# Performance work log

Hardware: AMD Instinct MI355X
Metric: run time of the kernel (lower is better)

The kernel has to match this reference:

```python
import jax, jax.numpy as jnp
import numpy as np

B, S, H, U = 32, 4096, 512, 512


def setup_inputs() -> dict:
    key = jax.random.key(0)
    ks = jax.random.split(key, 6)
    scale = 1.0 / np.sqrt(H)
    return {
        "query": jax.random.normal(ks[0], (B, H), dtype=jnp.float32),
        "values": jax.random.normal(ks[1], (B, S, H), dtype=jnp.float32),
        "W1": jax.random.normal(ks[2], (H, U), dtype=jnp.float32) * scale,
        "b1": jnp.zeros((U,), dtype=jnp.float32),
        "W2": jax.random.normal(ks[3], (H, U), dtype=jnp.float32) * scale,
        "b2": jnp.zeros((U,), dtype=jnp.float32),
        "va": jax.random.normal(ks[4], (U, 1), dtype=jnp.float32) * (1.0 / np.sqrt(U)),
        "bva": jnp.zeros((1,), dtype=jnp.float32),
    }


def reference(query, values, W1, b1, W2, b2, va, bva):
    # query: [B, H] -> [B, 1, U]; values: [B, S, H] -> [B, S, U]
    q_proj = jnp.einsum('bh,hu->bu', query, W1) + b1           # [B, U]
    v_proj = jnp.einsum('bsh,hu->bsu', values, W2) + b2        # [B, S, U]
    scores = jnp.einsum('bsu,uo->bso', jnp.tanh(q_proj[:, None, :] + v_proj), va) + bva  # [B, S, 1]
    attention_weights = jax.nn.softmax(scores, axis=1)         # [B, S, 1]
    context_vector = jnp.sum(attention_weights * values, axis=1)  # [B, H]
    return attention_weights, context_vector
```

## Files before the change

kernel.cpp:

```cpp
#include <hip/hip_runtime.h>
#include <hip/hip_bf16.h>
#include <stdint.h>

#define B_SZ 32
#define S_SZ 4096
#define H_SZ 512
#define U_SZ 512

typedef __attribute__((ext_vector_type(8))) _Float16 half8;
typedef __attribute__((ext_vector_type(4))) float floatx4;

__global__ __launch_bounds__(256) void prep_kernel(
    const float* __restrict__ W2, _Float16* __restrict__ W2s,
    float* __restrict__ qpb2, float* __restrict__ ctx)
{
    const int t = threadIdx.x;
    const int bid = blockIdx.x;
    const int i = bid * 256 + t;
    const int k = i >> 9, n = i & 511;
    W2s[(k >> 5) * 16384 + ((k >> 3) & 3) * 4096 + n * 8 + (k & 7)] =
        (_Float16)W2[i];
    if (bid < 64) qpb2[i] = 0.0f;
    else if (bid < 128) ctx[(bid - 64) * 256 + t] = 0.0f;
}

__global__ __launch_bounds__(256) void qproj_kernel(
    const float* __restrict__ query, const float* __restrict__ W1,
    const float* __restrict__ b1, const float* __restrict__ b2,
    float* __restrict__ qpb2)
{
    const int b = blockIdx.x, uc = blockIdx.y, ks = blockIdx.z;
    const int u = uc * 256 + threadIdx.x;
    const float* q  = query + b * H_SZ + ks * 64;
    const float* Wp = W1 + (size_t)(ks * 64) * U_SZ + u;
    float a0 = 0.f, a1 = 0.f, a2 = 0.f, a3 = 0.f;
    for (int k = 0; k < 64; k += 4) {
        a0 = fmaf(q[k],     Wp[(size_t)k * U_SZ],       a0);
        a1 = fmaf(q[k + 1], Wp[(size_t)(k + 1) * U_SZ], a1);
        a2 = fmaf(q[k + 2], Wp[(size_t)(k + 2) * U_SZ], a2);
        a3 = fmaf(q[k + 3], Wp[(size_t)(k + 3) * U_SZ], a3);
    }
    float acc = (a0 + a1) + (a2 + a3);
    if (ks == 0) acc += b1[u] + b2[u];
    atomicAdd(&qpb2[b * U_SZ + u], acc);
}

__global__ __launch_bounds__(256, 2) void scores_kernel(
    const float* __restrict__ values, const _Float16* __restrict__ W2s,
    const float* __restrict__ qpb2, const float* __restrict__ va,
    const float* __restrict__ bva, float* __restrict__ scores)
{
    __shared__ float red[256];

    const int t  = threadIdx.x;
    const int w  = t >> 6;
    const int l  = t & 63;
    const int c  = l & 15;
    const int g4 = l >> 4;
    const int m0 = blockIdx.x * 64;
    const int b  = m0 >> 12;

    floatx4 acc[4][8];
#pragma unroll
    for (int mt = 0; mt < 4; ++mt)
#pragma unroll
        for (int nt = 0; nt < 8; ++nt) acc[mt][nt] = (floatx4)(0.0f);

    const float* Ab = values + (size_t)(m0 + c) * H_SZ + g4 * 8;
    const _Float16* Bb = W2s + g4 * 4096 + (w * 128 + c) * 8;

    float4 an0[4], an1[4];
#pragma unroll
    for (int mt = 0; mt < 4; ++mt) {
        const float* ap = Ab + (size_t)(mt * 16) * H_SZ;
        an0[mt] = *(const float4*)(ap);
        an1[mt] = *(const float4*)(ap + 4);
    }
    half8 af[4];
#pragma unroll
    for (int mt = 0; mt < 4; ++mt) {
        half8 a;
        a[0] = (_Float16)an0[mt].x; a[1] = (_Float16)an0[mt].y;
        a[2] = (_Float16)an0[mt].z; a[3] = (_Float16)an0[mt].w;
        a[4] = (_Float16)an1[mt].x; a[5] = (_Float16)an1[mt].y;
        a[6] = (_Float16)an1[mt].z; a[7] = (_Float16)an1[mt].w;
        af[mt] = a;
    }

    for (int kb = 0; kb < 16; ++kb) {
        half8 bf[8];
        const _Float16* Bp = Bb + kb * 16384;
#pragma unroll
        for (int nt = 0; nt < 8; ++nt)
            bf[nt] = *(const half8*)(Bp + nt * 128);
        if (kb < 15) {
#pragma unroll
            for (int mt = 0; mt < 4; ++mt) {
                const float* ap = Ab + (size_t)(mt * 16) * H_SZ + (kb + 1) * 32;
                an0[mt] = *(const float4*)(ap);
                an1[mt] = *(const float4*)(ap + 4);
            }
        }
#pragma unroll
        for (int nt = 0; nt < 8; ++nt)
#pragma unroll
            for (int mt = 0; mt < 4; ++mt)
                acc[mt][nt] = __builtin_amdgcn_mfma_f32_16x16x32_f16(
                    af[mt], bf[nt], acc[mt][nt], 0, 0, 0);
        if (kb < 15) {
#pragma unroll
            for (int mt = 0; mt < 4; ++mt) {
                half8 a;
                a[0] = (_Float16)an0[mt].x; a[1] = (_Float16)an0[mt].y;
                a[2] = (_Float16)an0[mt].z; a[3] = (_Float16)an0[mt].w;
                a[4] = (_Float16)an1[mt].x; a[5] = (_Float16)an1[mt].y;
                a[6] = (_Float16)an1[mt].z; a[7] = (_Float16)an1[mt].w;
                af[mt] = a;
            }
        }
    }

    float qv2[8], vv[8], vv2[8];
#pragma unroll
    for (int nt = 0; nt < 8; ++nt) {
        const int n = w * 128 + nt * 16 + c;
        const float q = qpb2[b * U_SZ + n];
        const float v = va[n];
        qv2[nt] = 2.0f * q;
        vv[nt] = v;
        vv2[nt] = 2.0f * v;
    }
#pragma unroll
    for (int mt = 0; mt < 4; ++mt) {
#pragma unroll
        for (int r = 0; r < 4; ++r) {
            float p = 0.0f;
#pragma unroll
            for (int nt = 0; nt < 8; ++nt) {
                const float ex = __expf(fmaf(acc[mt][nt][r], 2.0f, qv2[nt]));
                const float rc = __builtin_amdgcn_rcpf(ex + 1.0f);
                p = fmaf(-vv2[nt], rc, p + vv[nt]);
            }
            p += __shfl_xor(p, 1);
            p += __shfl_xor(p, 2);
            p += __shfl_xor(p, 4);
            p += __shfl_xor(p, 8);
            if (c == 0) red[(mt * 16 + g4 * 4 + r) * 4 + w] = p;
        }
    }
    __syncthreads();
    if (t < 64)
        scores[m0 + t] = *bva + red[t * 4 + 0] + red[t * 4 + 1] +
                         red[t * 4 + 2] + red[t * 4 + 3];
}

__global__ __launch_bounds__(1024) void sredux_kernel(
    const float* __restrict__ scores, float* __restrict__ ML)
{
    __shared__ float red[16];
    __shared__ float s_max;
    const int b = blockIdx.x;
    const int t = threadIdx.x;
    float4 v = *(const float4*)(scores + b * S_SZ + t * 4);
    float m = fmaxf(fmaxf(v.x, v.y), fmaxf(v.z, v.w));
#pragma unroll
    for (int o = 32; o > 0; o >>= 1) m = fmaxf(m, __shfl_xor(m, o));
    if ((t & 63) == 0) red[t >> 6] = m;
    __syncthreads();
    if (t == 0) {
        float mm = red[0];
        for (int i = 1; i < 16; ++i) mm = fmaxf(mm, red[i]);
        s_max = mm;
    }
    __syncthreads();
    const float mm = s_max;
    float s = __expf(v.x - mm) + __expf(v.y - mm) +
              __expf(v.z - mm) + __expf(v.w - mm);
#pragma unroll
    for (int o = 32; o > 0; o >>= 1) s += __shfl_xor(s, o);
    if ((t & 63) == 0) red[t >> 6] = s;
    __syncthreads();
    if (t == 0) {
        float ss = 0.0f;
        for (int i = 0; i < 16; ++i) ss += red[i];
        ML[b * 2] = mm;
        ML[b * 2 + 1] = ss;
    }
}

__global__ __launch_bounds__(256) void context_kernel(
    const float* __restrict__ values, const float* __restrict__ scores,
    const float* __restrict__ ML, float* __restrict__ out)
{
    __shared__ float wl[128];
    __shared__ __align__(16) float part[4][64][4];
    const int ss = blockIdx.x, hc = blockIdx.y, b = blockIdx.z;
    const int t = threadIdx.x;
    const float M = ML[b * 2];
    const float rL = 1.0f / ML[b * 2 + 1];
    if (t < 32) {
        float4 sv = *(const float4*)(scores + b * S_SZ + ss * 128 + t * 4);
        float4 wv;
        wv.x = __expf(sv.x - M) * rL; wv.y = __expf(sv.y - M) * rL;
        wv.z = __expf(sv.z - M) * rL; wv.w = __expf(sv.w - M) * rL;
        *(float4*)&wl[t * 4] = wv;
        if (hc == 0)
            *(float4*)(out + b * S_SZ + ss * 128 + t * 4) = wv;
    }
    __syncthreads();

    const int l = t & 63, g = t >> 6;
    const float* vp = values + ((size_t)b * S_SZ + ss * 128 + g * 32) * H_SZ +
                      hc * 256 + l * 4;
    float4 a0 = {0,0,0,0}, a1 = {0,0,0,0}, a2 = {0,0,0,0}, a3 = {0,0,0,0};
    for (int i = 0; i < 32; i += 4) {
        const float w0 = wl[g * 32 + i];
        const float w1 = wl[g * 32 + i + 1];
        const float w2 = wl[g * 32 + i + 2];
        const float w3 = wl[g * 32 + i + 3];
        float4 v0 = *(const float4*)(vp + (size_t)(i)     * H_SZ);
        float4 v1 = *(const float4*)(vp + (size_t)(i + 1) * H_SZ);
        float4 v2 = *(const float4*)(vp + (size_t)(i + 2) * H_SZ);
        float4 v3 = *(const float4*)(vp + (size_t)(i + 3) * H_SZ);
        a0.x = fmaf(w0, v0.x, a0.x); a0.y = fmaf(w0, v0.y, a0.y);
        a0.z = fmaf(w0, v0.z, a0.z); a0.w = fmaf(w0, v0.w, a0.w);
        a1.x = fmaf(w1, v1.x, a1.x); a1.y = fmaf(w1, v1.y, a1.y);
        a1.z = fmaf(w1, v1.z, a1.z); a1.w = fmaf(w1, v1.w, a1.w);
        a2.x = fmaf(w2, v2.x, a2.x); a2.y = fmaf(w2, v2.y, a2.y);
        a2.z = fmaf(w2, v2.z, a2.z); a2.w = fmaf(w2, v2.w, a2.w);
        a3.x = fmaf(w3, v3.x, a3.x); a3.y = fmaf(w3, v3.y, a3.y);
        a3.z = fmaf(w3, v3.z, a3.z); a3.w = fmaf(w3, v3.w, a3.w);
    }
    a0.x += a1.x + a2.x + a3.x; a0.y += a1.y + a2.y + a3.y;
    a0.z += a1.z + a2.z + a3.z; a0.w += a1.w + a2.w + a3.w;
    *(float4*)&part[g][l][0] = a0;
    __syncthreads();
    if (t < 64) {
        float4 sa = *(float4*)&part[0][t][0];
#pragma unroll
        for (int gg = 1; gg < 4; ++gg) {
            float4 p = *(float4*)&part[gg][t][0];
            sa.x += p.x; sa.y += p.y; sa.z += p.z; sa.w += p.w;
        }
        float* ctx = out + B_SZ * S_SZ;
        const int hh = hc * 256 + t * 4;
        atomicAdd(&ctx[b * H_SZ + hh + 0], sa.x);
        atomicAdd(&ctx[b * H_SZ + hh + 1], sa.y);
        atomicAdd(&ctx[b * H_SZ + hh + 2], sa.z);
        atomicAdd(&ctx[b * H_SZ + hh + 3], sa.w);
    }
}

extern "C" void kernel_launch(void* const* d_in, const int* in_sizes, int n_in,
                              void* d_out, int out_size, void* d_ws, size_t ws_size,
                              hipStream_t stream) {
    const float* query  = (const float*)d_in[0];
    const float* values = (const float*)d_in[1];
    const float* W1     = (const float*)d_in[2];
    const float* b1     = (const float*)d_in[3];
    const float* W2     = (const float*)d_in[4];
    const float* b2     = (const float*)d_in[5];
    const float* va     = (const float*)d_in[6];
    const float* bva    = (const float*)d_in[7];
    float* out = (float*)d_out;

    char* ws = (char*)d_ws;
    float*    qpb2   = (float*)ws;
    _Float16* W2s    = (_Float16*)(ws + 65536);
    float*    scores = (float*)(ws + 65536 + 524288);
    float*    ML     = (float*)(ws + 65536 + 524288 + 524288);

    float* ctx = out + B_SZ * S_SZ;

    prep_kernel<<<1024, 256, 0, stream>>>(W2, W2s, qpb2, ctx);
    qproj_kernel<<<dim3(32, 2, 8), 256, 0, stream>>>(query, W1, b1, b2, qpb2);
    scores_kernel<<<2048, 256, 0, stream>>>(values, W2s, qpb2, va, bva, scores);
    sredux_kernel<<<32, 1024, 0, stream>>>(scores, ML);
    context_kernel<<<dim3(32, 2, 32), 256, 0, stream>>>(values, scores, ML, out);
}
```

Baseline: 618.0 us.

## Tile scores GEMM 128x128 with async LDS double buffering and fuse qproj

The scores GEMM now splits the unit dimension into four 128-wide tiles per block. Values and W2 tiles are staged into LDS with double-buffered async global-to-LDS copies, and per-tile partial scores are accumulated with atomics into a buffer pre-filled with bva. The query projection is merged into the prep kernel, which removes one launch and its atomics. The context kernel covers the full hidden dimension per block, halving the block count. In exchange, the values tensor is re-read once per unit tile, which adds global/L2 traffic, and scores now depend on atomic accumulation.

```diff
diff --git a/kernel.cpp b/kernel.cpp
--- a/kernel.cpp
+++ b/kernel.cpp
@@ -10,120 +10,128 @@
 typedef __attribute__((ext_vector_type(8))) _Float16 half8;
 typedef __attribute__((ext_vector_type(4))) float floatx4;
 
+__device__ __forceinline__ void async_copy16(const void* g, void* l) {
+    __builtin_amdgcn_global_load_lds(
+        (const __attribute__((address_space(1))) void*)g,
+        (__attribute__((address_space(3))) void*)l, 16, 0, 0);
+}
+
 __global__ __launch_bounds__(256) void prep_kernel(
-    const float* __restrict__ W2, _Float16* __restrict__ W2s,
-    float* __restrict__ qpb2, float* __restrict__ ctx)
+    const float* __restrict__ W2, const float* __restrict__ b1,
+    const float* __restrict__ b2, const float* __restrict__ bva,
+    const float* __restrict__ query, const float* __restrict__ W1,
+    _Float16* __restrict__ W2s, float* __restrict__ qpb2,
+    float* __restrict__ scores, float* __restrict__ ctx)
 {
     const int t = threadIdx.x;
     const int bid = blockIdx.x;
-    const int i = bid * 256 + t;
-    const int k = i >> 9, n = i & 511;
-    W2s[(k >> 5) * 16384 + ((k >> 3) & 3) * 4096 + n * 8 + (k & 7)] =
-        (_Float16)W2[i];
-    if (bid < 64) qpb2[i] = 0.0f;
-    else if (bid < 128) ctx[(bid - 64) * 256 + t] = 0.0f;
-}
-
-__global__ __launch_bounds__(256) void qproj_kernel(
-    const float* __restrict__ query, const float* __restrict__ W1,
-    const float* __restrict__ b1, const float* __restrict__ b2,
-    float* __restrict__ qpb2)
-{
-    const int b = blockIdx.x, uc = blockIdx.y, ks = blockIdx.z;
-    const int u = uc * 256 + threadIdx.x;
-    const float* q  = query + b * H_SZ + ks * 64;
-    const float* Wp = W1 + (size_t)(ks * 64) * U_SZ + u;
-    float a0 = 0.f, a1 = 0.f, a2 = 0.f, a3 = 0.f;
-    for (int k = 0; k < 64; k += 4) {
-        a0 = fmaf(q[k],     Wp[(size_t)k * U_SZ],       a0);
-        a1 = fmaf(q[k + 1], Wp[(size_t)(k + 1) * U_SZ], a1);
-        a2 = fmaf(q[k + 2], Wp[(size_t)(k + 2) * U_SZ], a2);
-        a3 = fmaf(q[k + 3], Wp[(size_t)(k + 3) * U_SZ], a3);
-    }
-    float acc = (a0 + a1) + (a2 + a3);
-    if (ks == 0) acc += b1[u] + b2[u];
-    atomicAdd(&qpb2[b * U_SZ + u], acc);
-}
-
-__global__ __launch_bounds__(256, 2) void scores_kernel(
+    if (bid < 1024) {
+        const int i = bid * 256 + t;
+        const int k = i >> 9, n = i & 511;
+        W2s[(k >> 5) * 16384 + ((k >> 3) & 3) * 4096 + n * 8 + (k & 7)] =
+            (_Float16)W2[i];
+    } else if (bid < 1536) {
+        scores[(bid - 1024) * 256 + t] = *bva;
+    } else if (bid < 1600) {
+        ctx[(bid - 1536) * 256 + t] = 0.0f;
+    } else {
+        const int bq = bid - 1600;
+        const int b = bq >> 1, uc = bq & 1;
+        const int u = uc * 256 + t;
+        const float* q  = query + b * H_SZ;
+        const float* Wp = W1 + u;
+        float a0 = 0.f, a1 = 0.f, a2 = 0.f, a3 = 0.f;
+        for (int k = 0; k < 512; k += 4) {
+            a0 = fmaf(q[k],     Wp[(size_t)k * U_SZ],       a0);
+            a1 = fmaf(q[k + 1], Wp[(size_t)(k + 1) * U_SZ], a1);
+            a2 = fmaf(q[k + 2], Wp[(size_t)(k + 2) * U_SZ], a2);
+            a3 = fmaf(q[k + 3], Wp[(size_t)(k + 3) * U_SZ], a3);
+        }
+        qpb2[b * U_SZ + u] = (a0 + a1) + (a2 + a3) + b1[u] + b2[u];
+    }
+}
+
+__global__ __launch_bounds__(256, 3) void scores_kernel(
     const float* __restrict__ values, const _Float16* __restrict__ W2s,
     const float* __restrict__ qpb2, const float* __restrict__ va,
-    const float* __restrict__ bva, float* __restrict__ scores)
-{
+    float* __restrict__ scores)
+{
+    __shared__ __align__(16) float    Albs[2][4096];
+    __shared__ __align__(16) _Float16 Blbs[2][4096];
     __shared__ float red[256];
 
     const int t  = threadIdx.x;
-    const int w  = t >> 6;
-    const int l  = t & 63;
-    const int c  = l & 15;
-    const int g4 = l >> 4;
-    const int m0 = blockIdx.x * 64;
+    const int w  = t >> 6, l = t & 63;
+    const int c  = l & 15, g4 = l >> 4;
+    const int mh = w >> 1, nh = w & 1;
+    const int n0 = (blockIdx.x & 3) * 128;
+    const int m0 = (blockIdx.x >> 2) * 128;
     const int b  = m0 >> 12;
 
-    floatx4 acc[4][8];
+    floatx4 acc[4][4];
 #pragma unroll
     for (int mt = 0; mt < 4; ++mt)
 #pragma unroll
-        for (int nt = 0; nt < 8; ++nt) acc[mt][nt] = (floatx4)(0.0f);
-
-    const float* Ab = values + (size_t)(m0 + c) * H_SZ + g4 * 8;
-    const _Float16* Bb = W2s + g4 * 4096 + (w * 128 + c) * 8;
-
-    float4 an0[4], an1[4];
-#pragma unroll
-    for (int mt = 0; mt < 4; ++mt) {
-        const float* ap = Ab + (size_t)(mt * 16) * H_SZ;
-        an0[mt] = *(const float4*)(ap);
-        an1[mt] = *(const float4*)(ap + 4);
-    }
-    half8 af[4];
-#pragma unroll
-    for (int mt = 0; mt < 4; ++mt) {
-        half8 a;
-        a[0] = (_Float16)an0[mt].x; a[1] = (_Float16)an0[mt].y;
-        a[2] = (_Float16)an0[mt].z; a[3] = (_Float16)an0[mt].w;
-        a[4] = (_Float16)an1[mt].x; a[5] = (_Float16)an1[mt].y;
-        a[6] = (_Float16)an1[mt].z; a[7] = (_Float16)an1[mt].w;
-        af[mt] = a;
-    }
+        for (int nt = 0; nt < 4; ++nt) acc[mt][nt] = (floatx4)(0.0f);
+
+    const float*    Vb0 = values + (size_t)m0 * H_SZ;
+    const _Float16* Wb0 = W2s + n0 * 8;
+
+    auto stage = [&](int kb, int buf) {
+        const float* Vb = Vb0 + kb * 32;
+#pragma unroll
+        for (int i = 0; i < 4; ++i) {
+            const int j = t + i * 256;
+            const int g = j >> 7, ml = j & 127;
+            async_copy16(Vb + (size_t)ml * H_SZ + g * 4, &Albs[buf][j * 4]);
+        }
+        const _Float16* Wb = Wb0 + kb * 16384;
+#pragma unroll
+        for (int i = 0; i < 2; ++i) {
+            const int j = t + i * 256;
+            const int kq = j >> 7, nl = j & 127;
+            async_copy16(Wb + kq * 4096 + nl * 8, &Blbs[buf][j * 8]);
+        }
+    };
+
+    stage(0, 0);
+    __syncthreads();
 
     for (int kb = 0; kb < 16; ++kb) {
-        half8 bf[8];
-        const _Float16* Bp = Bb + kb * 16384;
-#pragma unroll
-        for (int nt = 0; nt < 8; ++nt)
-            bf[nt] = *(const half8*)(Bp + nt * 128);
-        if (kb < 15) {
-#pragma unroll
-            for (int mt = 0; mt < 4; ++mt) {
-                const float* ap = Ab + (size_t)(mt * 16) * H_SZ + (kb + 1) * 32;
-                an0[mt] = *(const float4*)(ap);
-                an1[mt] = *(const float4*)(ap + 4);
-            }
-        }
-#pragma unroll
-        for (int nt = 0; nt < 8; ++nt)
-#pragma unroll
-            for (int mt = 0; mt < 4; ++mt)
+        const int cur = kb & 1;
+        if (kb < 15) stage(kb + 1, cur ^ 1);
+        half8 af[4];
+#pragma unroll
+        for (int mt = 0; mt < 4; ++mt) {
+            const int ml = mh * 64 + mt * 16 + c;
+            float4 lo = *(const float4*)&Albs[cur][((2 * g4)     * 128 + ml) * 4];
+            float4 hi = *(const float4*)&Albs[cur][((2 * g4 + 1) * 128 + ml) * 4];
+            half8 a;
+            a[0] = (_Float16)lo.x; a[1] = (_Float16)lo.y;
+            a[2] = (_Float16)lo.z; a[3] = (_Float16)lo.w;
+            a[4] = (_Float16)hi.x; a[5] = (_Float16)hi.y;
+            a[6] = (_Float16)hi.z; a[7] = (_Float16)hi.w;
+            af[mt] = a;
+        }
+        half8 bf[4];
+#pragma unroll
+        for (int nt = 0; nt < 4; ++nt) {
+            const int nl = nh * 64 + nt * 16 + c;
+            bf[nt] = *(const half8*)&Blbs[cur][(g4 * 128 + nl) * 8];
+        }
+#pragma unroll
+        for (int mt = 0; mt < 4; ++mt)
+#pragma unroll
+            for (int nt = 0; nt < 4; ++nt)
                 acc[mt][nt] = __builtin_amdgcn_mfma_f32_16x16x32_f16(
                     af[mt], bf[nt], acc[mt][nt], 0, 0, 0);
-        if (kb < 15) {
-#pragma unroll
-            for (int mt = 0; mt < 4; ++mt) {
-                half8 a;
-                a[0] = (_Float16)an0[mt].x; a[1] = (_Float16)an0[mt].y;
-                a[2] = (_Float16)an0[mt].z; a[3] = (_Float16)an0[mt].w;
-                a[4] = (_Float16)an1[mt].x; a[5] = (_Float16)an1[mt].y;
-                a[6] = (_Float16)an1[mt].z; a[7] = (_Float16)an1[mt].w;
-                af[mt] = a;
-            }
-        }
-    }
-
-    float qv2[8], vv[8], vv2[8];
-#pragma unroll
-    for (int nt = 0; nt < 8; ++nt) {
-        const int n = w * 128 + nt * 16 + c;
+        __syncthreads();
+    }
+
+    float qv2[4], vv[4], vv2[4];
+#pragma unroll
+    for (int nt = 0; nt < 4; ++nt) {
+        const int n = n0 + nh * 64 + nt * 16 + c;
         const float q = qpb2[b * U_SZ + n];
         const float v = va[n];
         qv2[nt] = 2.0f * q;
@@ -136,7 +144,7 @@
         for (int r = 0; r < 4; ++r) {
             float p = 0.0f;
 #pragma unroll
-            for (int nt = 0; nt < 8; ++nt) {
+            for (int nt = 0; nt < 4; ++nt) {
                 const float ex = __expf(fmaf(acc[mt][nt][r], 2.0f, qv2[nt]));
                 const float rc = __builtin_amdgcn_rcpf(ex + 1.0f);
                 p = fmaf(-vv2[nt], rc, p + vv[nt]);
@@ -145,13 +153,13 @@
             p += __shfl_xor(p, 2);
             p += __shfl_xor(p, 4);
             p += __shfl_xor(p, 8);
-            if (c == 0) red[(mt * 16 + g4 * 4 + r) * 4 + w] = p;
-        }
-    }
-    __syncthreads();
-    if (t < 64)
-        scores[m0 + t] = *bva + red[t * 4 + 0] + red[t * 4 + 1] +
-                         red[t * 4 + 2] + red[t * 4 + 3];
+            if (c == 0)
+                red[(mh * 64 + mt * 16 + g4 * 4 + r) * 2 + nh] = p;
+        }
+    }
+    __syncthreads();
+    if (t < 128)
+        atomicAdd(&scores[m0 + t], red[t * 2] + red[t * 2 + 1]);
 }
 
 __global__ __launch_bounds__(1024) void sredux_kernel(
@@ -193,61 +201,55 @@
     const float* __restrict__ ML, float* __restrict__ out)
 {
     __shared__ float wl[128];
-    __shared__ __align__(16) float part[4][64][4];
-    const int ss = blockIdx.x, hc = blockIdx.y, b = blockIdx.z;
+    __shared__ __align__(16) float part[4][512];
+    const int sc = blockIdx.x, b = blockIdx.y;
     const int t = threadIdx.x;
+    const int s0 = sc * 128;
     const float M = ML[b * 2];
     const float rL = 1.0f / ML[b * 2 + 1];
     if (t < 32) {
-        float4 sv = *(const float4*)(scores + b * S_SZ + ss * 128 + t * 4);
+        float4 sv = *(const float4*)(scores + b * S_SZ + s0 + t * 4);
         float4 wv;
         wv.x = __expf(sv.x - M) * rL; wv.y = __expf(sv.y - M) * rL;
         wv.z = __expf(sv.z - M) * rL; wv.w = __expf(sv.w - M) * rL;
         *(float4*)&wl[t * 4] = wv;
-        if (hc == 0)
-            *(float4*)(out + b * S_SZ + ss * 128 + t * 4) = wv;
-    }
-    __syncthreads();
-
-    const int l = t & 63, g = t >> 6;
-    const float* vp = values + ((size_t)b * S_SZ + ss * 128 + g * 32) * H_SZ +
-                      hc * 256 + l * 4;
-    float4 a0 = {0,0,0,0}, a1 = {0,0,0,0}, a2 = {0,0,0,0}, a3 = {0,0,0,0};
-    for (int i = 0; i < 32; i += 4) {
+        *(float4*)(out + b * S_SZ + s0 + t * 4) = wv;
+    }
+    __syncthreads();
+
+    const int g = t >> 6, l = t & 63;
+    const float* vp = values + ((size_t)b * S_SZ + s0 + g * 32) * H_SZ + l * 4;
+    float4 a00 = {0,0,0,0}, a01 = {0,0,0,0}, a10 = {0,0,0,0}, a11 = {0,0,0,0};
+    for (int i = 0; i < 32; i += 2) {
         const float w0 = wl[g * 32 + i];
         const float w1 = wl[g * 32 + i + 1];
-        const float w2 = wl[g * 32 + i + 2];
-        const float w3 = wl[g * 32 + i + 3];
-        float4 v0 = *(const float4*)(vp + (size_t)(i)     * H_SZ);
-        float4 v1 = *(const float4*)(vp + (size_t)(i + 1) * H_SZ);
-        float4 v2 = *(const float4*)(vp + (size_t)(i + 2) * H_SZ);
-        float4 v3 = *(const float4*)(vp + (size_t)(i + 3) * H_SZ);
-        a0.x = fmaf(w0, v0.x, a0.x); a0.y = fmaf(w0, v0.y, a0.y);
-        a0.z = fmaf(w0, v0.z, a0.z); a0.w = fmaf(w0, v0.w, a0.w);
-        a1.x = fmaf(w1, v1.x, a1.x); a1.y = fmaf(w1, v1.y, a1.y);
-        a1.z = fmaf(w1, v1.z, a1.z); a1.w = fmaf(w1, v1.w, a1.w);
-        a2.x = fmaf(w2, v2.x, a2.x); a2.y = fmaf(w2, v2.y, a2.y);
-        a2.z = fmaf(w2, v2.z, a2.z); a2.w = fmaf(w2, v2.w, a2.w);
-        a3.x = fmaf(w3, v3.x, a3.x); a3.y = fmaf(w3, v3.y, a3.y);
-        a3.z = fmaf(w3, v3.z, a3.z); a3.w = fmaf(w3, v3.w, a3.w);
-    }
-    a0.x += a1.x + a2.x + a3.x; a0.y += a1.y + a2.y + a3.y;
-    a0.z += a1.z + a2.z + a3.z; a0.w += a1.w + a2.w + a3.w;
-    *(float4*)&part[g][l][0] = a0;
-    __syncthreads();
-    if (t < 64) {
-        float4 sa = *(float4*)&part[0][t][0];
-#pragma unroll
-        for (int gg = 1; gg < 4; ++gg) {
-            float4 p = *(float4*)&part[gg][t][0];
-            sa.x += p.x; sa.y += p.y; sa.z += p.z; sa.w += p.w;
-        }
-        float* ctx = out + B_SZ * S_SZ;
-        const int hh = hc * 256 + t * 4;
-        atomicAdd(&ctx[b * H_SZ + hh + 0], sa.x);
-        atomicAdd(&ctx[b * H_SZ + hh + 1], sa.y);
-        atomicAdd(&ctx[b * H_SZ + hh + 2], sa.z);
-        atomicAdd(&ctx[b * H_SZ + hh + 3], sa.w);
+        const float* r0 = vp + (size_t)i * H_SZ;
+        const float* r1 = r0 + H_SZ;
+        float4 v00 = *(const float4*)(r0);
+        float4 v01 = *(const float4*)(r0 + 256);
+        float4 v10 = *(const float4*)(r1);
+        float4 v11 = *(const float4*)(r1 + 256);
+        a00.x = fmaf(w0, v00.x, a00.x); a00.y = fmaf(w0, v00.y, a00.y);
+        a00.z = fmaf(w0, v00.z, a00.z); a00.w = fmaf(w0, v00.w, a00.w);
+        a01.x = fmaf(w0, v01.x, a01.x); a01.y = fmaf(w0, v01.y, a01.y);
+        a01.z = fmaf(w0, v01.z, a01.z); a01.w = fmaf(w0, v01.w, a01.w);
+        a10.x = fmaf(w1, v10.x, a10.x); a10.y = fmaf(w1, v10.y, a10.y);
+        a10.z = fmaf(w1, v10.z, a10.z); a10.w = fmaf(w1, v10.w, a10.w);
+        a11.x = fmaf(w1, v11.x, a11.x); a11.y = fmaf(w1, v11.y, a11.y);
+        a11.z = fmaf(w1, v11.z, a11.z); a11.w = fmaf(w1, v11.w, a11.w);
+    }
+    a00.x += a10.x; a00.y += a10.y; a00.z += a10.z; a00.w += a10.w;
+    a01.x += a11.x; a01.y += a11.y; a01.z += a11.z; a01.w += a11.w;
+    *(float4*)&part[g][l * 4] = a00;
+    *(float4*)&part[g][256 + l * 4] = a01;
+    __syncthreads();
+
+    float* ctx = out + B_SZ * S_SZ;
+#pragma unroll
+    for (int rep = 0; rep < 2; ++rep) {
+        const int h = rep * 256 + t;
+        const float s = (part[0][h] + part[1][h]) + (part[2][h] + part[3][h]);
+        atomicAdd(&ctx[b * H_SZ + h], s);
     }
 }
 
@@ -268,13 +270,13 @@
     float*    qpb2   = (float*)ws;
     _Float16* W2s    = (_Float16*)(ws + 65536);
     float*    scores = (float*)(ws + 65536 + 524288);
-    float*    ML     = (float*)(ws + 65536 + 524288 + 524288);
+    float*    ML     = (float*)(ws + 65536 + 2 * 524288);
 
     float* ctx = out + B_SZ * S_SZ;
 
-    prep_kernel<<<1024, 256, 0, stream>>>(W2, W2s, qpb2, ctx);
-    qproj_kernel<<<dim3(32, 2, 8), 256, 0, stream>>>(query, W1, b1, b2, qpb2);
-    scores_kernel<<<2048, 256, 0, stream>>>(values, W2s, qpb2, va, bva, scores);
+    prep_kernel<<<1664, 256, 0, stream>>>(W2, b1, b2, bva, query, W1,
+                                          W2s, qpb2, scores, ctx);
+    scores_kernel<<<4096, 256, 0, stream>>>(values, W2s, qpb2, va, scores);
     sredux_kernel<<<32, 1024, 0, stream>>>(scores, ML);
-    context_kernel<<<dim3(32, 2, 32), 256, 0, stream>>>(values, scores, ML, out);
-}
+    context_kernel<<<dim3(32, 32), 256, 0, stream>>>(values, scores, ML, out);
+}
```

New measurement: 595.9 us. 3.6% less time.
